# Kernel tuning notes

Measured on AMD Instinct MI355X. Metric: run time of the kernel, lower is better.

## Reference

```python
import jax, jax.numpy as jnp
import numpy as np

AUX_LOSS_ALPHA = 0.01
TOP_K = 2
N_EXPERTS = 64


def setup_inputs() -> dict:
    key = jax.random.key(0)
    k1, k2 = jax.random.split(key)
    B, S, H, E = 4, 4096, 2048, N_EXPERTS
    hidden_states = jax.random.normal(k1, (B, S, H), dtype=jnp.float32)
    # kaiming_uniform_(a=sqrt(5)) ~ U(-1/sqrt(H), 1/sqrt(H))
    bound = 1.0 / np.sqrt(H)
    weight = jax.random.uniform(k2, (E, H), dtype=jnp.float32, minval=-bound, maxval=bound)
    return {"hidden_states": hidden_states, "weight": weight}


def reference(hidden_states, weight):
    B, S, H = hidden_states.shape
    E, K = N_EXPERTS, TOP_K
    x = hidden_states.reshape(-1, H)              # [T, H], T = B*S
    logits = jnp.einsum('th,eh->te', x, weight)   # router GEMM [T, E]
    scores = jax.nn.softmax(logits, axis=-1)
    topk_weight, topk_idx = jax.lax.top_k(scores, K)  # [T, K]
    # norm_topk_prob (K > 1)
    topk_weight = topk_weight / (jnp.sum(topk_weight, axis=-1, keepdims=True) + 1e-20)
    # seq_aux auxiliary loss (training path)
    idx2d = topk_idx.reshape(B, S * K)            # [B, S*K]
    ce = jnp.zeros((B, E), dtype=scores.dtype)
    ce = ce.at[jnp.arange(B)[:, None], idx2d].add(1.0)
    ce = ce / (S * K / E)
    scores3 = scores.reshape(B, S, E)
    aux_loss = jnp.mean(jnp.sum(ce * jnp.mean(scores3, axis=1), axis=1)) * AUX_LOSS_ALPHA
    return topk_idx, topk_weight, aux_loss
```

## Files before the change

kernel.cpp:

```cpp
#include <hip/hip_runtime.h>
#include <math.h>


#define TT 16384
#define HH 2048
#define EE 64
#define BB 4
#define M_TOK 16
#define KCH 256
#define TAU 2e-3f
#define NBLK (TT / M_TOK)

typedef float v4f __attribute__((ext_vector_type(4)));
typedef float f4v __attribute__((ext_vector_type(4)));
typedef short s8v __attribute__((ext_vector_type(8)));

__device__ __forceinline__ unsigned short f2bf(float f) {
    unsigned u = __float_as_uint(f);
    return (unsigned short)((u + 0x7fffu + ((u >> 16) & 1u)) >> 16);
}
__device__ __forceinline__ float bf2f(unsigned short h) {
    return __uint_as_float(((unsigned)h) << 16);
}

__global__ void prep_b(const float* __restrict__ w,
                       unsigned short* __restrict__ bhi,
                       unsigned short* __restrict__ blo,
                       int* __restrict__ done) {
    if (blockIdx.x == 0 && threadIdx.x == 0)
        __hip_atomic_store(done, 0, __ATOMIC_RELAXED, __HIP_MEMORY_SCOPE_AGENT);
    int idx = blockIdx.x * blockDim.x + threadIdx.x;
    int j    = idx & 7;
    int lane = (idx >> 3) & 63;
    int ks   = (idx >> 9) & 63;
    int nt   = idx >> 15;
    int e = nt * 16 + (lane & 15);
    int k = ks * 32 + (lane >> 4) * 8 + j;
    float f = w[e * HH + k];
    unsigned short h = f2bf(f);
    bhi[idx] = h;
    blo[idx] = f2bf(f - bf2f(h));
}

__global__ __launch_bounds__(256) void gemm_gate(
    const float* __restrict__ x,
    const unsigned short* __restrict__ bhi, const unsigned short* __restrict__ blo,
    const float* __restrict__ w,
    float* __restrict__ out_idx, float* __restrict__ out_w,
    float* __restrict__ part, int* __restrict__ done,
    float* __restrict__ aux_out) {

    __shared__ unsigned short ahi[2][8 * 64 * 8];
    __shared__ unsigned short alo[2][8 * 64 * 8];
    __shared__ float lg[M_TOK][68];
    __shared__ float bssum[EE];
    __shared__ float bcnt[EE];
    __shared__ int   fl[M_TOK];
    __shared__ int   fl_cnt;
    __shared__ int   lastf;
    __shared__ float warpsum[4];

    const int tid  = threadIdx.x;
    const int wave = tid >> 6;
    const int lane = tid & 63;
    const int tok0 = blockIdx.x * M_TOK;
    const int m  = tid >> 4;
    const int kb = tid & 15;

    if (tid < EE) { bssum[tid] = 0.f; bcnt[tid] = 0.f; }
    if (tid == 0) fl_cnt = 0;

    v4f rx[2][4];

    auto LD = [&](int c, int s) {
        const float* __restrict__ xp = x + (size_t)(tok0 + m) * HH + c * KCH + kb * 8;
        rx[s][0] = *(const v4f*)xp;
        rx[s][1] = *(const v4f*)(xp + 4);
        rx[s][2] = *(const v4f*)(xp + 128);
        rx[s][3] = *(const v4f*)(xp + 132);
    };
    auto ST = [&](int s, int bi) {
#pragma unroll
        for (int g = 0; g < 2; ++g) {
            v4f a = rx[s][g * 2], b2 = rx[s][g * 2 + 1];
            float xs[8] = {a.x, a.y, a.z, a.w, b2.x, b2.y, b2.z, b2.w};
            s8v hv, lv;
#pragma unroll
            for (int j = 0; j < 8; ++j) {
                unsigned short h = f2bf(xs[j]);
                hv[j] = (short)h;
                lv[j] = (short)f2bf(xs[j] - bf2f(h));
            }
            const int k8i = kb + g * 16;
            const int kstep = k8i >> 2, quad = k8i & 3;
            const int entry = kstep * 64 + quad * 16 + (m ^ (quad << 1));
            *(s8v*)&ahi[bi][entry * 8] = hv;
            *(s8v*)&alo[bi][entry * 8] = lv;
        }
    };

    LD(0, 0);
    LD(1, 1);
    ST(0, 0);
    __syncthreads();

    f4v acc = {0.f, 0.f, 0.f, 0.f};
    const int rdl = lane ^ ((lane >> 4) << 1);

#pragma unroll
    for (int c = 0; c < 8; ++c) {
        const int cur = c & 1;
        if (c < 6) LD(c + 2, cur);
        if (c < 7) ST(cur ^ 1, cur ^ 1);
#pragma unroll
        for (int ks = 0; ks < 8; ++ks) {
            const int entry = ks * 64 + rdl;
            s8v af_h = *(const s8v*)&ahi[cur][entry * 8];
            s8v af_l = *(const s8v*)&alo[cur][entry * 8];
            const size_t boff = ((size_t)(wave * 64 + c * 8 + ks) * 64 + lane) * 8;
            s8v bf_h = *(const s8v*)&bhi[boff];
            s8v bf_l = *(const s8v*)&blo[boff];
            acc = __builtin_amdgcn_mfma_f32_16x16x32_bf16(af_h, bf_h, acc, 0, 0, 0);
            acc = __builtin_amdgcn_mfma_f32_16x16x32_bf16(af_h, bf_l, acc, 0, 0, 0);
            acc = __builtin_amdgcn_mfma_f32_16x16x32_bf16(af_l, bf_h, acc, 0, 0, 0);
        }
        __syncthreads();
    }

#pragma unroll
    for (int r = 0; r < 4; ++r) {
        const int row = (lane >> 4) * 4 + r;
        const int col = wave * 16 + (lane & 15);
        lg[row][col] = acc[r];
    }
    __syncthreads();

    float ssum_l = 0.f;

#pragma unroll
    for (int r = 0; r < 4; ++r) {
        const int tl = wave * 4 + r;
        const int t  = tok0 + tl;
        float l = lg[tl][lane];

        float mx = l;
#pragma unroll
        for (int off = 32; off; off >>= 1) mx = fmaxf(mx, __shfl_xor(mx, off, 64));
        float p = __expf(l - mx);
        float Z = p;
#pragma unroll
        for (int off = 32; off; off >>= 1) Z += __shfl_xor(Z, off, 64);
        ssum_l += p / Z;

        float v = l;
        int cand[3]; float cl[3];
#pragma unroll
        for (int q = 0; q < 3; ++q) {
            float bv = v; int bi = lane;
#pragma unroll
            for (int off = 32; off; off >>= 1) {
                float ov = __shfl_xor(bv, off, 64);
                int   oi = __shfl_xor(bi, off, 64);
                if (ov > bv || (ov == bv && oi < bi)) { bv = ov; bi = oi; }
            }
            cand[q] = bi; cl[q] = bv;
            if (lane == bi) v = -3.4e38f;
        }

        if (lane == 0) {
            atomicAdd(&bcnt[cand[0]], 1.f);
            atomicAdd(&bcnt[cand[1]], 1.f);
            float w1 = 1.f / (1.f + __expf(cl[1] - cl[0]));
            out_idx[t * 2]     = (float)cand[0];
            out_idx[t * 2 + 1] = (float)cand[1];
            out_w[t * 2]       = w1;
            out_w[t * 2 + 1]   = 1.f - w1;
            if (cl[0] - cl[1] < TAU || cl[1] - cl[2] < TAU) {
                int pos = atomicAdd(&fl_cnt, 1);
                fl[pos] = tl;
            }
        }
    }

    atomicAdd(&bssum[lane], ssum_l);
    __syncthreads();

    if (tid < 128) {
        float vv = (tid < 64) ? bcnt[tid] : bssum[tid - 64];
        __hip_atomic_store(&part[(size_t)blockIdx.x * 128 + tid], vv,
                           __ATOMIC_RELAXED, __HIP_MEMORY_SCOPE_AGENT);
    }
    __syncthreads();
    if (tid == 0) {
        int old = __hip_atomic_fetch_add(done, 1, __ATOMIC_ACQ_REL,
                                         __HIP_MEMORY_SCOPE_AGENT);
        lastf = (old == NBLK - 1) ? 1 : 0;
    }

    const int nfl = fl_cnt;
    for (int i = wave; i < nfl; i += 4) {
        const int tl = fl[i];
        const int t  = tok0 + tl;
        float l = lg[tl][lane];

        float v = l;
        int cand4[4];
#pragma unroll
        for (int q = 0; q < 4; ++q) {
            float bv = v; int bi = lane;
#pragma unroll
            for (int off = 32; off; off >>= 1) {
                float ov = __shfl_xor(bv, off, 64);
                int   oi = __shfl_xor(bi, off, 64);
                if (ov > bv || (ov == bv && oi < bi)) { bv = ov; bi = oi; }
            }
            cand4[q] = bi;
            if (lane == bi) v = -3.4e38f;
        }

        const float* __restrict__ xt  = x + (size_t)t * HH;
        const float* __restrict__ w0p = w + (size_t)cand4[0] * HH;
        const float* __restrict__ w1p = w + (size_t)cand4[1] * HH;
        const float* __restrict__ w2p = w + (size_t)cand4[2] * HH;
        const float* __restrict__ w3p = w + (size_t)cand4[3] * HH;
        double d0 = 0.0, d1 = 0.0, d2 = 0.0, d3 = 0.0;
#pragma unroll
        for (int ii = 0; ii < 8; ++ii) {
            const int k = ii * 256 + lane * 4;
            v4f xv = *(const v4f*)(xt + k);
            v4f a0 = *(const v4f*)(w0p + k);
            v4f a1 = *(const v4f*)(w1p + k);
            v4f a2 = *(const v4f*)(w2p + k);
            v4f a3 = *(const v4f*)(w3p + k);
            double dx0 = (double)xv.x, dx1 = (double)xv.y;
            double dx2 = (double)xv.z, dx3 = (double)xv.w;
            d0 = fma(dx0, (double)a0.x, d0); d0 = fma(dx1, (double)a0.y, d0);
            d0 = fma(dx2, (double)a0.z, d0); d0 = fma(dx3, (double)a0.w, d0);
            d1 = fma(dx0, (double)a1.x, d1); d1 = fma(dx1, (double)a1.y, d1);
            d1 = fma(dx2, (double)a1.z, d1); d1 = fma(dx3, (double)a1.w, d1);
            d2 = fma(dx0, (double)a2.x, d2); d2 = fma(dx1, (double)a2.y, d2);
            d2 = fma(dx2, (double)a2.z, d2); d2 = fma(dx3, (double)a2.w, d2);
            d3 = fma(dx0, (double)a3.x, d3); d3 = fma(dx1, (double)a3.y, d3);
            d3 = fma(dx2, (double)a3.z, d3); d3 = fma(dx3, (double)a3.w, d3);
        }
#pragma unroll
        for (int off = 32; off; off >>= 1) {
            d0 += __shfl_xor(d0, off, 64);
            d1 += __shfl_xor(d1, off, 64);
            d2 += __shfl_xor(d2, off, 64);
            d3 += __shfl_xor(d3, off, 64);
        }

        double bd[4] = {d0, d1, d2, d3};
        int e1 = cand4[0]; double l1 = bd[0];
#pragma unroll
        for (int q = 1; q < 4; ++q)
            if (bd[q] > l1 || (bd[q] == l1 && cand4[q] < e1)) { l1 = bd[q]; e1 = cand4[q]; }
        int e2 = -1; double l2 = -1e300;
#pragma unroll
        for (int q = 0; q < 4; ++q) {
            if (cand4[q] == e1) continue;
            if (e2 < 0 || bd[q] > l2 || (bd[q] == l2 && cand4[q] < e2)) { l2 = bd[q]; e2 = cand4[q]; }
        }

        double w1d = 1.0 / (1.0 + exp(l2 - l1));
        if (lane == 0) {
            out_idx[t * 2]     = (float)e1;
            out_idx[t * 2 + 1] = (float)e2;
            out_w[t * 2]       = (float)w1d;
            out_w[t * 2 + 1]   = (float)(1.0 - w1d);
        }
    }

    __syncthreads();
    if (!lastf) return;

    {
        const int b = tid >> 6, e = tid & 63;
        float cnt = 0.f, ssum = 0.f;
        for (int blk = b * 256; blk < (b + 1) * 256; ++blk) {
            cnt  += __hip_atomic_load(&part[(size_t)blk * 128 + e],
                                      __ATOMIC_RELAXED, __HIP_MEMORY_SCOPE_AGENT);
            ssum += __hip_atomic_load(&part[(size_t)blk * 128 + 64 + e],
                                      __ATOMIC_RELAXED, __HIP_MEMORY_SCOPE_AGENT);
        }
        float a = cnt * ssum;
#pragma unroll
        for (int off = 32; off; off >>= 1) a += __shfl_xor(a, off, 64);
        if ((tid & 63) == 0) warpsum[tid >> 6] = a;
        __syncthreads();
        if (tid == 0)
            aux_out[0] = (warpsum[0] + warpsum[1] + warpsum[2] + warpsum[3])
                         * (0.01f / (4.f * 128.f * 4096.f));
    }
}

extern "C" void kernel_launch(void* const* d_in, const int* in_sizes, int n_in,
                              void* d_out, int out_size, void* d_ws, size_t ws_size,
                              hipStream_t stream) {
    const float* x = (const float*)d_in[0];
    const float* w = (const float*)d_in[1];
    float* out = (float*)d_out;
    float* out_idx = out;
    float* out_w   = out + 2 * TT;
    float* aux     = out + 4 * TT;

    unsigned short* bhi = (unsigned short*)d_ws;
    unsigned short* blo = bhi + (size_t)EE * HH;
    float* part = (float*)(blo + (size_t)EE * HH);
    int*   done = (int*)(part + (size_t)NBLK * 128);

    prep_b<<<(EE * HH) / 256, 256, 0, stream>>>(w, bhi, blo, done);
    gemm_gate<<<NBLK, 256, 0, stream>>>(x, bhi, blo, w, out_idx, out_w,
                                        part, done, aux);
}
```

Measured before the change: 254.9 us.

## Replace last-block reduction with replicated global atomics and a finalize kernel

Each block now atomically adds its per-expert counts and score sums into 8 replicated global accumulators, replacing the per-block partial stores and the done-counter handshake. The last-block serial reduction over 1024 partials moves into a separate tiny finalize kernel. This removes the acq_rel counter atomic and the long tail loop in one block. In exchange it adds a third kernel launch and contended float atomics.

```diff
diff --git a/kernel.cpp b/kernel.cpp
--- a/kernel.cpp
+++ b/kernel.cpp
@@ -9,6 +9,7 @@
 #define M_TOK 16
 #define KCH 256
 #define TAU 2e-3f
+#define NREP 8
 #define NBLK (TT / M_TOK)
 
 typedef float v4f __attribute__((ext_vector_type(4)));
@@ -26,9 +27,10 @@
 __global__ void prep_b(const float* __restrict__ w,
                        unsigned short* __restrict__ bhi,
                        unsigned short* __restrict__ blo,
-                       int* __restrict__ done) {
-    if (blockIdx.x == 0 && threadIdx.x == 0)
-        __hip_atomic_store(done, 0, __ATOMIC_RELAXED, __HIP_MEMORY_SCOPE_AGENT);
+                       float* __restrict__ zreg) {
+    if (blockIdx.x == 0) {
+        for (int i = threadIdx.x; i < 2 * NREP * BB * EE; i += 256) zreg[i] = 0.f;
+    }
     int idx = blockIdx.x * blockDim.x + threadIdx.x;
     int j    = idx & 7;
     int lane = (idx >> 3) & 63;
@@ -47,8 +49,7 @@
     const unsigned short* __restrict__ bhi, const unsigned short* __restrict__ blo,
     const float* __restrict__ w,
     float* __restrict__ out_idx, float* __restrict__ out_w,
-    float* __restrict__ part, int* __restrict__ done,
-    float* __restrict__ aux_out) {
+    float* __restrict__ g_cnt, float* __restrict__ g_ssum) {
 
     __shared__ unsigned short ahi[2][8 * 64 * 8];
     __shared__ unsigned short alo[2][8 * 64 * 8];
@@ -57,8 +58,6 @@
     __shared__ float bcnt[EE];
     __shared__ int   fl[M_TOK];
     __shared__ int   fl_cnt;
-    __shared__ int   lastf;
-    __shared__ float warpsum[4];
 
     const int tid  = threadIdx.x;
     const int wave = tid >> 6;
@@ -185,16 +184,13 @@
     atomicAdd(&bssum[lane], ssum_l);
     __syncthreads();
 
-    if (tid < 128) {
-        float vv = (tid < 64) ? bcnt[tid] : bssum[tid - 64];
-        __hip_atomic_store(&part[(size_t)blockIdx.x * 128 + tid], vv,
-                           __ATOMIC_RELAXED, __HIP_MEMORY_SCOPE_AGENT);
-    }
-    __syncthreads();
-    if (tid == 0) {
-        int old = __hip_atomic_fetch_add(done, 1, __ATOMIC_ACQ_REL,
-                                         __HIP_MEMORY_SCOPE_AGENT);
-        lastf = (old == NBLK - 1) ? 1 : 0;
+    {
+        const int b   = tok0 >> 12;
+        const int rep = (blockIdx.x & (NREP - 1)) * (BB * EE);
+        if (tid < EE)
+            atomicAdd(&g_cnt[rep + b * EE + tid], bcnt[tid]);
+        else if (tid < 2 * EE)
+            atomicAdd(&g_ssum[rep + b * EE + (tid - EE)], bssum[tid - EE]);
     }
 
     const int nfl = fl_cnt;
@@ -271,28 +267,25 @@
             out_w[t * 2 + 1]   = (float)(1.0 - w1d);
         }
     }
-
-    __syncthreads();
-    if (!lastf) return;
-
-    {
-        const int b = tid >> 6, e = tid & 63;
-        float cnt = 0.f, ssum = 0.f;
-        for (int blk = b * 256; blk < (b + 1) * 256; ++blk) {
-            cnt  += __hip_atomic_load(&part[(size_t)blk * 128 + e],
-                                      __ATOMIC_RELAXED, __HIP_MEMORY_SCOPE_AGENT);
-            ssum += __hip_atomic_load(&part[(size_t)blk * 128 + 64 + e],
-                                      __ATOMIC_RELAXED, __HIP_MEMORY_SCOPE_AGENT);
-        }
-        float a = cnt * ssum;
-#pragma unroll
-        for (int off = 32; off; off >>= 1) a += __shfl_xor(a, off, 64);
-        if ((tid & 63) == 0) warpsum[tid >> 6] = a;
-        __syncthreads();
-        if (tid == 0)
-            aux_out[0] = (warpsum[0] + warpsum[1] + warpsum[2] + warpsum[3])
-                         * (0.01f / (4.f * 128.f * 4096.f));
-    }
+}
+
+__global__ void finalize(const float* __restrict__ g_cnt,
+                         const float* __restrict__ g_ssum,
+                         float* __restrict__ aux_out) {
+    int lane = threadIdx.x;
+    float a = 0.f;
+    for (int b = 0; b < BB; ++b) {
+        float c = 0.f, ss = 0.f;
+#pragma unroll
+        for (int r = 0; r < NREP; ++r) {
+            c  += g_cnt[r * (BB * EE) + b * EE + lane];
+            ss += g_ssum[r * (BB * EE) + b * EE + lane];
+        }
+        a += c * ss;
+    }
+#pragma unroll
+    for (int off = 32; off; off >>= 1) a += __shfl_xor(a, off, 64);
+    if (lane == 0) aux_out[0] = a * (0.01f / (4.f * 128.f * 4096.f));
 }
 
 extern "C" void kernel_launch(void* const* d_in, const int* in_sizes, int n_in,
@@ -307,10 +300,11 @@
 
     unsigned short* bhi = (unsigned short*)d_ws;
     unsigned short* blo = bhi + (size_t)EE * HH;
-    float* part = (float*)(blo + (size_t)EE * HH);
-    int*   done = (int*)(part + (size_t)NBLK * 128);
-
-    prep_b<<<(EE * HH) / 256, 256, 0, stream>>>(w, bhi, blo, done);
+    float* g_cnt  = (float*)(blo + (size_t)EE * HH);
+    float* g_ssum = g_cnt + NREP * BB * EE;
+
+    prep_b<<<(EE * HH) / 256, 256, 0, stream>>>(w, bhi, blo, g_cnt);
     gemm_gate<<<NBLK, 256, 0, stream>>>(x, bhi, blo, w, out_idx, out_w,
-                                        part, done, aux);
-}
+                                        g_cnt, g_ssum);
+    finalize<<<1, 64, 0, stream>>>(g_cnt, g_ssum, aux);
+}
```

After: 219.6 us. -13.8%, faster.
